# Performance work log

Measured on AMD Instinct MI355X. Metric: run time of the kernel, lower is better.

## Reference

```python
import jax, jax.numpy as jnp
import numpy as np

S, B, D, DV = 2048, 16, 128, 128


def setup_inputs() -> dict:
    key = jax.random.key(0)
    kq, kk, kv = jax.random.split(key, 3)
    return {
        "query": jax.random.normal(kq, (S, B, D), dtype=jnp.float32),
        "key": jax.random.normal(kk, (S, B, D), dtype=jnp.float32),
        "value": jax.random.normal(kv, (S, B, DV), dtype=jnp.float32),
    }


def reference(query, key, value):
    # sim: [B, S_q, S_k]
    d = key.shape[-1]
    sim = jnp.einsum('sbd,tbd->bst', query, key) / jnp.sqrt(jnp.asarray(d, query.dtype))
    # causal mask: disallow attending to future positions (strictly upper triangle)
    sq, sk = sim.shape[-2], sim.shape[-1]
    causal = jnp.tril(jnp.ones((sq, sk), dtype=bool))  # [S_q, S_k]
    sim = jnp.where(causal[None, :, :], sim, -jnp.inf)
    a = jax.nn.softmax(sim, axis=-1)  # dropout omitted (eval mode, p=0)
    # context: [S_q, B, D_v]
    context = jnp.einsum('bst,tbe->sbe', a, value)
    return context
```

## Files before the change

### kernel.cpp

```cpp
#include <hip/hip_runtime.h>
#include <stdint.h>

#define SS 2048
#define BB 16
#define DD 128
#define DVV 128
#define BQ 32
#define BK 32
#define NTILES (SS / BK)
#define TILE_HW 4096

typedef __attribute__((ext_vector_type(8))) short short8;
typedef __attribute__((ext_vector_type(4))) float float4v;

typedef __attribute__((address_space(1))) const void glob_cv;
typedef __attribute__((address_space(3))) void lds_v;

__device__ __forceinline__ short f2bf(float f) {
  union { float f; uint32_t u; } x;
  x.f = f;
  uint32_t r = x.u + 0x7fffu + ((x.u >> 16) & 1u);
  return (short)(r >> 16);
}
__device__ __forceinline__ float bf2f(short h) {
  union { uint32_t u; float f; } y;
  y.u = ((uint32_t)(uint16_t)h) << 16;
  return y.f;
}

__device__ __forceinline__ int kappa(int quad, int j) {
  return (j < 4) ? (quad * 4 + j) : (16 + quad * 4 + (j - 4));
}

__global__ __launch_bounds__(256) void conv_kv(
    const float* __restrict__ kg, const float* __restrict__ vg,
    short* __restrict__ kimg, short* __restrict__ vimg) {
  __shared__ short tile[BK][136];
  const int t = blockIdx.x, b = blockIdx.y;
  if (blockIdx.z == 0) {
    short* out = kimg + ((size_t)(b * NTILES + t)) * TILE_HW;
#pragma unroll
    for (int p = 0; p < 2; ++p) {
      const int ch = threadIdx.x + p * 256;
      const int key = ch >> 4, c = ch & 15;
      const float* src = kg + ((size_t)(t * BK + key) * BB + b) * DD + c * 8;
      float4v f0 = *(const float4v*)src;
      float4v f1 = *(const float4v*)(src + 4);
      short8 s;
#pragma unroll
      for (int i = 0; i < 4; ++i) { s[i] = f2bf(f0[i]); s[4 + i] = f2bf(f1[i]); }
      *(short8*)(out + key * 128 + ((c ^ (key & 7)) * 8)) = s;
    }
  } else {
    short* out = vimg + ((size_t)(b * NTILES + t)) * TILE_HW;
#pragma unroll
    for (int p = 0; p < 2; ++p) {
      const int ch = threadIdx.x + p * 256;
      const int key = ch >> 4, fc = ch & 15;
      const float* src = vg + ((size_t)(t * BK + key) * BB + b) * DVV + fc * 8;
      float4v f0 = *(const float4v*)src;
      float4v f1 = *(const float4v*)(src + 4);
      short8 s;
#pragma unroll
      for (int i = 0; i < 4; ++i) { s[i] = f2bf(f0[i]); s[4 + i] = f2bf(f1[i]); }
      *(short8*)&tile[key][fc * 8] = s;
    }
    __syncthreads();
#pragma unroll
    for (int p = 0; p < 2; ++p) {
      const int idx = threadIdx.x + p * 256;
      const int nt = idx >> 6, quad = (idx >> 4) & 3, mm = idx & 15;
      const int dv = nt * 16 + mm;
      short8 s;
#pragma unroll
      for (int j = 0; j < 8; ++j) s[j] = tile[kappa(quad, j)][dv];
      *(short8*)(out + idx * 8) = s;
    }
  }
}

__global__ __launch_bounds__(128) void attn_fwd(
    const float* __restrict__ qg, const short* __restrict__ kimg,
    const short* __restrict__ vimg, float* __restrict__ og) {
  __shared__ __align__(16) short kbuf[2][TILE_HW];
  __shared__ __align__(16) short vbuf[2][TILE_HW];

  const int tid  = threadIdx.x;
  const int wave = tid >> 6;
  const int lane = tid & 63;
  const int m    = lane & 15;
  const int quad = lane >> 4;
  const int bid  = blockIdx.x;
  const int half = bid >> 9, idx = bid & 511;
  const int qt   = half ? (idx >> 4) : (63 - (idx >> 4));
  const int b    = idx & 15;
  const int qw   = qt * BQ + wave * 16;
  const int qrow = qw + m;

  const float cscale = 0.08838834764831845f * 1.4426950408889634f;
  short8 qfrag[4];
#pragma unroll
  for (int ks = 0; ks < 4; ++ks) {
    const float* qp = qg + ((size_t)qrow * BB + b) * DD + ks * 32 + quad * 8;
    float4v f0 = *(const float4v*)qp;
    float4v f1 = *(const float4v*)(qp + 4);
    short8 f;
#pragma unroll
    for (int i = 0; i < 4; ++i) { f[i] = f2bf(f0[i] * cscale); f[4 + i] = f2bf(f1[i] * cscale); }
    qfrag[ks] = f;
  }

  float4v oacc[8];
#pragma unroll
  for (int i = 0; i < 8; ++i) oacc[i] = (float4v){0.f, 0.f, 0.f, 0.f};
  float psum = 0.f;

  const short* tsrc = (wave ? vimg : kimg) + (size_t)b * NTILES * TILE_HW + lane * 8;
  short* const dst0 = wave ? vbuf[0] : kbuf[0];
  short* const dst1 = wave ? vbuf[1] : kbuf[1];

  const int ntile = qt + 1;
#pragma unroll
  for (int j = 0; j < 8; ++j)
    __builtin_amdgcn_global_load_lds((glob_cv*)(tsrc + j * 512),
                                     (lds_v*)(dst0 + j * 512), 16, 0, 0);

  for (int t = 0; t < ntile; ++t) {
    const int par = t & 1;
    __syncthreads();
    if (t + 1 < ntile) {
      const short* src = tsrc + (size_t)(t + 1) * TILE_HW;
      short* dst = par ? dst0 : dst1;
#pragma unroll
      for (int j = 0; j < 8; ++j)
        __builtin_amdgcn_global_load_lds((glob_cv*)(src + j * 512),
                                         (lds_v*)(dst + j * 512), 16, 0, 0);
    }
    const short* kb = kbuf[par];
    const short* vb = vbuf[par];

    float4v s0 = {0.f, 0.f, 0.f, 0.f}, s1 = {0.f, 0.f, 0.f, 0.f};
#pragma unroll
    for (int ks = 0; ks < 4; ++ks) {
      const int c = ks * 4 + quad;
      short8 kf0 = *(const short8*)&kb[m * 128 + ((c ^ (m & 7)) * 8)];
      short8 kf1 = *(const short8*)&kb[(16 + m) * 128 + ((c ^ (m & 7)) * 8)];
      s0 = __builtin_amdgcn_mfma_f32_16x16x32_bf16(kf0, qfrag[ks], s0, 0, 0, 0);
      s1 = __builtin_amdgcn_mfma_f32_16x16x32_bf16(kf1, qfrag[ks], s1, 0, 0, 0);
    }
    float sv[8];
#pragma unroll
    for (int r = 0; r < 4; ++r) { sv[r] = s0[r]; sv[4 + r] = s1[r]; }

    const int kt0 = t * BK;
    if (kt0 + BK - 1 > qw) {
#pragma unroll
      for (int j = 0; j < 8; ++j)
        if (kt0 + kappa(quad, j) > qrow) sv[j] = -1e30f;
    }

    short8 pfrag;
#pragma unroll
    for (int j = 0; j < 8; ++j) {
      float p = exp2f(sv[j]);
      short h = f2bf(p);
      pfrag[j] = h;
      psum += bf2f(h);
    }

#pragma unroll
    for (int nt = 0; nt < 8; ++nt) {
      short8 vf = *(const short8*)&vb[nt * 512 + lane * 8];
      oacc[nt] = __builtin_amdgcn_mfma_f32_16x16x32_bf16(pfrag, vf, oacc[nt], 0, 0, 0);
    }
  }

  float l = psum;
  l += __shfl_xor(l, 16, 64);
  l += __shfl_xor(l, 32, 64);
  const float linv = 1.0f / l;
  float l4[4];
#pragma unroll
  for (int r = 0; r < 4; ++r) l4[r] = __shfl(linv, quad * 4 + r, 64);
#pragma unroll
  for (int r = 0; r < 4; ++r) {
    const int qgl = qw + quad * 4 + r;
    float* op = og + ((size_t)qgl * BB + b) * DVV + m;
#pragma unroll
    for (int nt = 0; nt < 8; ++nt) op[nt * 16] = oacc[nt][r] * l4[r];
  }
}

extern "C" void kernel_launch(void* const* d_in, const int* in_sizes, int n_in,
                              void* d_out, int out_size, void* d_ws, size_t ws_size,
                              hipStream_t stream) {
  const float* q = (const float*)d_in[0];
  const float* k = (const float*)d_in[1];
  const float* v = (const float*)d_in[2];
  float* out = (float*)d_out;
  short* kimg = (short*)d_ws;
  short* vimg = kimg + (size_t)BB * NTILES * TILE_HW;

  conv_kv<<<dim3(NTILES, BB, 2), 256, 0, stream>>>(k, v, kimg, vimg);
  attn_fwd<<<dim3(SS / BQ * BB), 128, 0, stream>>>(q, kimg, vimg, out);
}
```

Measured before the change: 141.3 us.

## Split key tiles across two wave pairs with LDS reduction of partial outputs

```diff
diff --git a/kernel.cpp b/kernel.cpp
--- a/kernel.cpp
+++ b/kernel.cpp
@@ -79,22 +79,25 @@
   }
 }
 
-__global__ __launch_bounds__(128) void attn_fwd(
+__global__ __launch_bounds__(256) void attn_fwd(
     const float* __restrict__ qg, const short* __restrict__ kimg,
     const short* __restrict__ vimg, float* __restrict__ og) {
-  __shared__ __align__(16) short kbuf[2][TILE_HW];
-  __shared__ __align__(16) short vbuf[2][TILE_HW];
-
-  const int tid  = threadIdx.x;
-  const int wave = tid >> 6;
-  const int lane = tid & 63;
-  const int m    = lane & 15;
-  const int quad = lane >> 4;
-  const int bid  = blockIdx.x;
+  __shared__ __align__(16) short smem[4 * TILE_HW];
+  short* const sKb = smem;
+  short* const sVb = smem + 2 * TILE_HW;
+
+  const int tid   = threadIdx.x;
+  const int wave  = tid >> 6;
+  const int qwave = wave & 1;
+  const int tpar  = wave >> 1;
+  const int lane  = tid & 63;
+  const int m     = lane & 15;
+  const int quad  = lane >> 4;
+  const int bid   = blockIdx.x;
   const int half = bid >> 9, idx = bid & 511;
   const int qt   = half ? (idx >> 4) : (63 - (idx >> 4));
   const int b    = idx & 15;
-  const int qw   = qt * BQ + wave * 16;
+  const int qw   = qt * BQ + qwave * 16;
   const int qrow = qw + m;
 
   const float cscale = 0.08838834764831845f * 1.4426950408889634f;
@@ -115,79 +118,94 @@
   for (int i = 0; i < 8; ++i) oacc[i] = (float4v){0.f, 0.f, 0.f, 0.f};
   float psum = 0.f;
 
-  const short* tsrc = (wave ? vimg : kimg) + (size_t)b * NTILES * TILE_HW + lane * 8;
-  short* const dst0 = wave ? vbuf[0] : kbuf[0];
-  short* const dst1 = wave ? vbuf[1] : kbuf[1];
-
-  const int ntile = qt + 1;
-#pragma unroll
-  for (int j = 0; j < 8; ++j)
-    __builtin_amdgcn_global_load_lds((glob_cv*)(tsrc + j * 512),
-                                     (lds_v*)(dst0 + j * 512), 16, 0, 0);
-
-  for (int t = 0; t < ntile; ++t) {
-    const int par = t & 1;
+  const short* tsrc = (qwave ? vimg : kimg) + (size_t)b * NTILES * TILE_HW + lane * 8;
+  short* const sdst = (qwave ? sVb : sKb) + tpar * TILE_HW;
+
+  const int ntile  = qt + 1;
+  const int nround = (ntile + 1) >> 1;
+
+  for (int r = 0; r < nround; ++r) {
+    const int t = 2 * r + tpar;
     __syncthreads();
-    if (t + 1 < ntile) {
-      const short* src = tsrc + (size_t)(t + 1) * TILE_HW;
-      short* dst = par ? dst0 : dst1;
+    if (t < ntile) {
+      const short* src = tsrc + (size_t)t * TILE_HW;
 #pragma unroll
       for (int j = 0; j < 8; ++j)
         __builtin_amdgcn_global_load_lds((glob_cv*)(src + j * 512),
-                                         (lds_v*)(dst + j * 512), 16, 0, 0);
-    }
-    const short* kb = kbuf[par];
-    const short* vb = vbuf[par];
-
-    float4v s0 = {0.f, 0.f, 0.f, 0.f}, s1 = {0.f, 0.f, 0.f, 0.f};
-#pragma unroll
-    for (int ks = 0; ks < 4; ++ks) {
-      const int c = ks * 4 + quad;
-      short8 kf0 = *(const short8*)&kb[m * 128 + ((c ^ (m & 7)) * 8)];
-      short8 kf1 = *(const short8*)&kb[(16 + m) * 128 + ((c ^ (m & 7)) * 8)];
-      s0 = __builtin_amdgcn_mfma_f32_16x16x32_bf16(kf0, qfrag[ks], s0, 0, 0, 0);
-      s1 = __builtin_amdgcn_mfma_f32_16x16x32_bf16(kf1, qfrag[ks], s1, 0, 0, 0);
-    }
-    float sv[8];
-#pragma unroll
-    for (int r = 0; r < 4; ++r) { sv[r] = s0[r]; sv[4 + r] = s1[r]; }
-
-    const int kt0 = t * BK;
-    if (kt0 + BK - 1 > qw) {
-#pragma unroll
-      for (int j = 0; j < 8; ++j)
-        if (kt0 + kappa(quad, j) > qrow) sv[j] = -1e30f;
-    }
-
-    short8 pfrag;
-#pragma unroll
-    for (int j = 0; j < 8; ++j) {
-      float p = exp2f(sv[j]);
-      short h = f2bf(p);
-      pfrag[j] = h;
-      psum += bf2f(h);
-    }
-
-#pragma unroll
-    for (int nt = 0; nt < 8; ++nt) {
-      short8 vf = *(const short8*)&vb[nt * 512 + lane * 8];
-      oacc[nt] = __builtin_amdgcn_mfma_f32_16x16x32_bf16(pfrag, vf, oacc[nt], 0, 0, 0);
-    }
-  }
-
-  float l = psum;
-  l += __shfl_xor(l, 16, 64);
-  l += __shfl_xor(l, 32, 64);
-  const float linv = 1.0f / l;
-  float l4[4];
-#pragma unroll
-  for (int r = 0; r < 4; ++r) l4[r] = __shfl(linv, quad * 4 + r, 64);
-#pragma unroll
-  for (int r = 0; r < 4; ++r) {
-    const int qgl = qw + quad * 4 + r;
-    float* op = og + ((size_t)qgl * BB + b) * DVV + m;
-#pragma unroll
-    for (int nt = 0; nt < 8; ++nt) op[nt * 16] = oacc[nt][r] * l4[r];
+                                         (lds_v*)(sdst + j * 512), 16, 0, 0);
+    }
+    __syncthreads();
+
+    if (t < ntile) {
+      const short* kb = sKb + tpar * TILE_HW;
+      const short* vb = sVb + tpar * TILE_HW;
+
+      float4v s0 = {0.f, 0.f, 0.f, 0.f}, s1 = {0.f, 0.f, 0.f, 0.f};
+#pragma unroll
+      for (int ks = 0; ks < 4; ++ks) {
+        const int c = ks * 4 + quad;
+        short8 kf0 = *(const short8*)&kb[m * 128 + ((c ^ (m & 7)) * 8)];
+        short8 kf1 = *(const short8*)&kb[(16 + m) * 128 + ((c ^ (m & 7)) * 8)];
+        s0 = __builtin_amdgcn_mfma_f32_16x16x32_bf16(kf0, qfrag[ks], s0, 0, 0, 0);
+        s1 = __builtin_amdgcn_mfma_f32_16x16x32_bf16(kf1, qfrag[ks], s1, 0, 0, 0);
+      }
+      float sv[8];
+#pragma unroll
+      for (int rr = 0; rr < 4; ++rr) { sv[rr] = s0[rr]; sv[4 + rr] = s1[rr]; }
+
+      const int kt0 = t * BK;
+      if (kt0 + BK - 1 > qw) {
+#pragma unroll
+        for (int j = 0; j < 8; ++j)
+          if (kt0 + kappa(quad, j) > qrow) sv[j] = -1e30f;
+      }
+
+      short8 pfrag;
+#pragma unroll
+      for (int j = 0; j < 8; ++j) {
+        float p = exp2f(sv[j]);
+        short h = f2bf(p);
+        pfrag[j] = h;
+        psum += bf2f(h);
+      }
+
+#pragma unroll
+      for (int nt = 0; nt < 8; ++nt) {
+        short8 vf = *(const short8*)&vb[nt * 512 + lane * 8];
+        oacc[nt] = __builtin_amdgcn_mfma_f32_16x16x32_bf16(pfrag, vf, oacc[nt], 0, 0, 0);
+      }
+    }
+  }
+
+  __syncthreads();
+  float* const cw = (float*)smem;
+  if (tpar == 1) {
+    float* p = cw + (size_t)(qwave * 64 + lane) * 36;
+#pragma unroll
+    for (int nt = 0; nt < 8; ++nt) *(float4v*)(p + nt * 4) = oacc[nt];
+    p[32] = psum;
+  }
+  __syncthreads();
+  if (tpar == 0) {
+    const float* p = cw + (size_t)(qwave * 64 + lane) * 36;
+#pragma unroll
+    for (int nt = 0; nt < 8; ++nt) oacc[nt] += *(const float4v*)(p + nt * 4);
+    psum += p[32];
+
+    float l = psum;
+    l += __shfl_xor(l, 16, 64);
+    l += __shfl_xor(l, 32, 64);
+    const float linv = 1.0f / l;
+    float l4[4];
+#pragma unroll
+    for (int rr = 0; rr < 4; ++rr) l4[rr] = __shfl(linv, quad * 4 + rr, 64);
+#pragma unroll
+    for (int rr = 0; rr < 4; ++rr) {
+      const int qgl = qw + quad * 4 + rr;
+      float* op = og + ((size_t)qgl * BB + b) * DVV + m;
+#pragma unroll
+      for (int nt = 0; nt < 8; ++nt) op[nt * 16] = oacc[nt][rr] * l4[rr];
+    }
   }
 }
 
@@ -202,5 +220,5 @@
   short* vimg = kimg + (size_t)BB * NTILES * TILE_HW;
 
   conv_kv<<<dim3(NTILES, BB, 2), 256, 0, stream>>>(k, v, kimg, vimg);
-  attn_fwd<<<dim3(SS / BQ * BB), 128, 0, stream>>>(q, kimg, vimg, out);
-}
+  attn_fwd<<<dim3(SS / BQ * BB), 256, 0, stream>>>(q, kimg, vimg, out);
+}
```

Result: faster. 135.4 us (-4.2%).

## Split KV tiles across four waves per block and reduce partial outputs in LDS

Applied to the files above, without the earlier changes.

```diff
diff --git a/kernel.cpp b/kernel.cpp
--- a/kernel.cpp
+++ b/kernel.cpp
@@ -79,115 +79,166 @@
   }
 }
 
-__global__ __launch_bounds__(128) void attn_fwd(
+__global__ __launch_bounds__(256) void attn_fwd(
     const float* __restrict__ qg, const short* __restrict__ kimg,
     const short* __restrict__ vimg, float* __restrict__ og) {
-  __shared__ __align__(16) short kbuf[2][TILE_HW];
-  __shared__ __align__(16) short vbuf[2][TILE_HW];
+  __shared__ __align__(16) short smem[8 * TILE_HW];
 
   const int tid  = threadIdx.x;
-  const int wave = tid >> 6;
+  const int tpar = tid >> 6;
   const int lane = tid & 63;
   const int m    = lane & 15;
   const int quad = lane >> 4;
   const int bid  = blockIdx.x;
-  const int half = bid >> 9, idx = bid & 511;
-  const int qt   = half ? (idx >> 4) : (63 - (idx >> 4));
-  const int b    = idx & 15;
-  const int qw   = qt * BQ + wave * 16;
-  const int qrow = qw + m;
+  const int qt   = (NTILES - 1) - (bid >> 4);
+  const int b    = bid & 15;
+  const int q0   = qt * BQ;
+  const int qrowA = q0 + m;
+  const int qrowB = q0 + 16 + m;
 
   const float cscale = 0.08838834764831845f * 1.4426950408889634f;
-  short8 qfrag[4];
+  short8 qfragA[4], qfragB[4];
 #pragma unroll
   for (int ks = 0; ks < 4; ++ks) {
-    const float* qp = qg + ((size_t)qrow * BB + b) * DD + ks * 32 + quad * 8;
-    float4v f0 = *(const float4v*)qp;
-    float4v f1 = *(const float4v*)(qp + 4);
-    short8 f;
-#pragma unroll
-    for (int i = 0; i < 4; ++i) { f[i] = f2bf(f0[i] * cscale); f[4 + i] = f2bf(f1[i] * cscale); }
-    qfrag[ks] = f;
-  }
-
-  float4v oacc[8];
-#pragma unroll
-  for (int i = 0; i < 8; ++i) oacc[i] = (float4v){0.f, 0.f, 0.f, 0.f};
-  float psum = 0.f;
-
-  const short* tsrc = (wave ? vimg : kimg) + (size_t)b * NTILES * TILE_HW + lane * 8;
-  short* const dst0 = wave ? vbuf[0] : kbuf[0];
-  short* const dst1 = wave ? vbuf[1] : kbuf[1];
+    const float* qpA = qg + ((size_t)qrowA * BB + b) * DD + ks * 32 + quad * 8;
+    const float* qpB = qg + ((size_t)qrowB * BB + b) * DD + ks * 32 + quad * 8;
+    float4v a0 = *(const float4v*)qpA, a1 = *(const float4v*)(qpA + 4);
+    float4v b0 = *(const float4v*)qpB, b1 = *(const float4v*)(qpB + 4);
+    short8 fa, fb;
+#pragma unroll
+    for (int i = 0; i < 4; ++i) {
+      fa[i] = f2bf(a0[i] * cscale); fa[4 + i] = f2bf(a1[i] * cscale);
+      fb[i] = f2bf(b0[i] * cscale); fb[4 + i] = f2bf(b1[i] * cscale);
+    }
+    qfragA[ks] = fa; qfragB[ks] = fb;
+  }
+
+  float4v oaccA[8], oaccB[8];
+#pragma unroll
+  for (int i = 0; i < 8; ++i) {
+    oaccA[i] = (float4v){0.f, 0.f, 0.f, 0.f};
+    oaccB[i] = (float4v){0.f, 0.f, 0.f, 0.f};
+  }
+  float psumA = 0.f, psumB = 0.f;
+
+  short* const kb = smem + tpar * TILE_HW;
+  short* const vb = smem + (4 + tpar) * TILE_HW;
+  const short* ksrc = kimg + (size_t)b * NTILES * TILE_HW + lane * 8;
+  const short* vsrc = vimg + (size_t)b * NTILES * TILE_HW + lane * 8;
 
   const int ntile = qt + 1;
-#pragma unroll
-  for (int j = 0; j < 8; ++j)
-    __builtin_amdgcn_global_load_lds((glob_cv*)(tsrc + j * 512),
-                                     (lds_v*)(dst0 + j * 512), 16, 0, 0);
-
-  for (int t = 0; t < ntile; ++t) {
-    const int par = t & 1;
-    __syncthreads();
-    if (t + 1 < ntile) {
-      const short* src = tsrc + (size_t)(t + 1) * TILE_HW;
-      short* dst = par ? dst0 : dst1;
-#pragma unroll
-      for (int j = 0; j < 8; ++j)
-        __builtin_amdgcn_global_load_lds((glob_cv*)(src + j * 512),
-                                         (lds_v*)(dst + j * 512), 16, 0, 0);
-    }
-    const short* kb = kbuf[par];
-    const short* vb = vbuf[par];
-
-    float4v s0 = {0.f, 0.f, 0.f, 0.f}, s1 = {0.f, 0.f, 0.f, 0.f};
+  for (int t = tpar; t < ntile; t += 4) {
+    __builtin_amdgcn_s_waitcnt(0x0000);
+    {
+      const short* sk = ksrc + (size_t)t * TILE_HW;
+      const short* sv2 = vsrc + (size_t)t * TILE_HW;
+#pragma unroll
+      for (int j = 0; j < 8; ++j) {
+        __builtin_amdgcn_global_load_lds((glob_cv*)(sk + j * 512),
+                                         (lds_v*)(kb + j * 512), 16, 0, 0);
+        __builtin_amdgcn_global_load_lds((glob_cv*)(sv2 + j * 512),
+                                         (lds_v*)(vb + j * 512), 16, 0, 0);
+      }
+    }
+    __builtin_amdgcn_s_waitcnt(0x0F70);
+
+    float4v sA0 = {0.f,0.f,0.f,0.f}, sA1 = {0.f,0.f,0.f,0.f};
+    float4v sB0 = {0.f,0.f,0.f,0.f}, sB1 = {0.f,0.f,0.f,0.f};
 #pragma unroll
     for (int ks = 0; ks < 4; ++ks) {
       const int c = ks * 4 + quad;
       short8 kf0 = *(const short8*)&kb[m * 128 + ((c ^ (m & 7)) * 8)];
       short8 kf1 = *(const short8*)&kb[(16 + m) * 128 + ((c ^ (m & 7)) * 8)];
-      s0 = __builtin_amdgcn_mfma_f32_16x16x32_bf16(kf0, qfrag[ks], s0, 0, 0, 0);
-      s1 = __builtin_amdgcn_mfma_f32_16x16x32_bf16(kf1, qfrag[ks], s1, 0, 0, 0);
-    }
-    float sv[8];
-#pragma unroll
-    for (int r = 0; r < 4; ++r) { sv[r] = s0[r]; sv[4 + r] = s1[r]; }
+      sA0 = __builtin_amdgcn_mfma_f32_16x16x32_bf16(kf0, qfragA[ks], sA0, 0, 0, 0);
+      sA1 = __builtin_amdgcn_mfma_f32_16x16x32_bf16(kf1, qfragA[ks], sA1, 0, 0, 0);
+      sB0 = __builtin_amdgcn_mfma_f32_16x16x32_bf16(kf0, qfragB[ks], sB0, 0, 0, 0);
+      sB1 = __builtin_amdgcn_mfma_f32_16x16x32_bf16(kf1, qfragB[ks], sB1, 0, 0, 0);
+    }
+    float svA[8], svB[8];
+#pragma unroll
+    for (int r = 0; r < 4; ++r) {
+      svA[r] = sA0[r]; svA[4 + r] = sA1[r];
+      svB[r] = sB0[r]; svB[4 + r] = sB1[r];
+    }
 
     const int kt0 = t * BK;
-    if (kt0 + BK - 1 > qw) {
+    if (kt0 + BK - 1 > q0) {
 #pragma unroll
       for (int j = 0; j < 8; ++j)
-        if (kt0 + kappa(quad, j) > qrow) sv[j] = -1e30f;
-    }
-
-    short8 pfrag;
+        if (kt0 + kappa(quad, j) > qrowA) svA[j] = -1e30f;
+    }
+    if (kt0 + BK - 1 > q0 + 16) {
+#pragma unroll
+      for (int j = 0; j < 8; ++j)
+        if (kt0 + kappa(quad, j) > qrowB) svB[j] = -1e30f;
+    }
+
+    short8 pfragA, pfragB;
 #pragma unroll
     for (int j = 0; j < 8; ++j) {
-      float p = exp2f(sv[j]);
-      short h = f2bf(p);
-      pfrag[j] = h;
-      psum += bf2f(h);
+      float pA = exp2f(svA[j]);
+      float pB = exp2f(svB[j]);
+      short hA = f2bf(pA), hB = f2bf(pB);
+      pfragA[j] = hA; pfragB[j] = hB;
+      psumA += bf2f(hA); psumB += bf2f(hB);
     }
 
 #pragma unroll
     for (int nt = 0; nt < 8; ++nt) {
       short8 vf = *(const short8*)&vb[nt * 512 + lane * 8];
-      oacc[nt] = __builtin_amdgcn_mfma_f32_16x16x32_bf16(pfrag, vf, oacc[nt], 0, 0, 0);
-    }
-  }
-
-  float l = psum;
-  l += __shfl_xor(l, 16, 64);
-  l += __shfl_xor(l, 32, 64);
-  const float linv = 1.0f / l;
-  float l4[4];
-#pragma unroll
-  for (int r = 0; r < 4; ++r) l4[r] = __shfl(linv, quad * 4 + r, 64);
-#pragma unroll
-  for (int r = 0; r < 4; ++r) {
-    const int qgl = qw + quad * 4 + r;
-    float* op = og + ((size_t)qgl * BB + b) * DVV + m;
-#pragma unroll
-    for (int nt = 0; nt < 8; ++nt) op[nt * 16] = oacc[nt][r] * l4[r];
+      oaccA[nt] = __builtin_amdgcn_mfma_f32_16x16x32_bf16(pfragA, vf, oaccA[nt], 0, 0, 0);
+      oaccB[nt] = __builtin_amdgcn_mfma_f32_16x16x32_bf16(pfragB, vf, oaccB[nt], 0, 0, 0);
+    }
+  }
+
+  __syncthreads();
+  float* const cw = (float*)smem;
+  if (tpar != 0) {
+    float* p = cw + (size_t)((tpar - 1) * 64 + lane) * 67;
+#pragma unroll
+    for (int nt = 0; nt < 8; ++nt) {
+      *(float4v*)(p + nt * 4)      = oaccA[nt];
+      *(float4v*)(p + 32 + nt * 4) = oaccB[nt];
+    }
+    p[64] = psumA;
+    p[65] = psumB;
+  }
+  __syncthreads();
+  if (tpar == 0) {
+#pragma unroll
+    for (int w = 0; w < 3; ++w) {
+      const float* p = cw + (size_t)(w * 64 + lane) * 67;
+#pragma unroll
+      for (int nt = 0; nt < 8; ++nt) {
+        oaccA[nt] += *(const float4v*)(p + nt * 4);
+        oaccB[nt] += *(const float4v*)(p + 32 + nt * 4);
+      }
+      psumA += p[64];
+      psumB += p[65];
+    }
+
+    float lA = psumA, lB = psumB;
+    lA += __shfl_xor(lA, 16, 64); lA += __shfl_xor(lA, 32, 64);
+    lB += __shfl_xor(lB, 16, 64); lB += __shfl_xor(lB, 32, 64);
+    const float liA = 1.0f / lA, liB = 1.0f / lB;
+    float l4A[4], l4B[4];
+#pragma unroll
+    for (int rr = 0; rr < 4; ++rr) {
+      l4A[rr] = __shfl(liA, quad * 4 + rr, 64);
+      l4B[rr] = __shfl(liB, quad * 4 + rr, 64);
+    }
+#pragma unroll
+    for (int rr = 0; rr < 4; ++rr) {
+      const int gA = q0 + quad * 4 + rr;
+      const int gB = q0 + 16 + quad * 4 + rr;
+      float* opA = og + ((size_t)gA * BB + b) * DVV + m;
+      float* opB = og + ((size_t)gB * BB + b) * DVV + m;
+#pragma unroll
+      for (int nt = 0; nt < 8; ++nt) {
+        opA[nt * 16] = oaccA[nt][rr] * l4A[rr];
+        opB[nt * 16] = oaccB[nt][rr] * l4B[rr];
+      }
+    }
   }
 }
 
@@ -202,5 +253,5 @@
   short* vimg = kimg + (size_t)BB * NTILES * TILE_HW;
 
   conv_kv<<<dim3(NTILES, BB, 2), 256, 0, stream>>>(k, v, kimg, vimg);
-  attn_fwd<<<dim3(SS / BQ * BB), 128, 0, stream>>>(q, kimg, vimg, out);
-}
+  attn_fwd<<<dim3(SS / BQ * BB), 256, 0, stream>>>(q, kimg, vimg, out);
+}
```

Result: no change. 140.8 us (-0.4%).
